# Kernel tuning notes

Measured on AMD Instinct MI355X. Metric: run time of the kernel, lower is better.

## Reference

```python
import jax, jax.numpy as jnp
import numpy as np

N, E = 50000, 1_600_000
IN_DIM, OUT_DIM, E_IN, E_OUT = 128, 64, 32, 32


def setup_inputs() -> dict:
    key = jax.random.key(0)
    ks = jax.random.split(key, 8)
    h = jax.random.normal(ks[0], (N, IN_DIM), jnp.float32)
    edge_w = jax.random.normal(ks[1], (E, E_IN), jnp.float32)
    src = jax.random.randint(ks[2], (E,), 0, N)
    dst = jax.random.randint(ks[3], (E,), 0, N)

    def winit(k, shape):
        fan_in = shape[0]
        return jax.random.normal(k, shape, jnp.float32) / np.float32(np.sqrt(fan_in))

    W_node = winit(ks[4], (IN_DIM, OUT_DIM))
    W_attn = winit(ks[5], (2 * OUT_DIM + E_IN, 1))
    W_tonode = winit(ks[6], (OUT_DIM + E_IN, OUT_DIM))
    W_edge = winit(ks[7], (2 * OUT_DIM + E_IN, E_OUT))
    return dict(h=h, edge_w=edge_w, W_node=W_node, W_attn=W_attn,
                W_tonode=W_tonode, W_edge=W_edge, src=src, dst=dst)


def reference(h, edge_w, W_node, W_attn, W_tonode, W_edge, src, dst):
    n = h.shape[0]
    d = W_node.shape[1]

    # embed_node
    z = h @ W_node                      # [N, D]
    zs = z[src]                         # [E, D] gather (message source feats)
    zd = z[dst]                         # [E, D]

    # edge_attention: attn_fc(cat[src, dst, w]) == split-matmul sum (no concat)
    a = zs @ W_attn[:d] + zd @ W_attn[d:2 * d] + edge_w @ W_attn[2 * d:]  # [E,1]
    e = jax.nn.leaky_relu(a, negative_slope=0.1)[:, 0]                    # [E]

    # segment softmax over incoming edges of each dst node
    emax = jax.lax.stop_gradient(jax.ops.segment_max(e, dst, num_segments=n))
    ex = jnp.exp(e - emax[dst])
    denom = jax.ops.segment_sum(ex, dst, num_segments=n)
    alpha = ex / denom[dst]             # [E]

    # to_node_fc(cat[src_h, w]) then alpha-weighted segment sum
    t = zs @ W_tonode[:d] + edge_w @ W_tonode[d:]         # [E, D]
    h_agg = jax.ops.segment_sum(alpha[:, None] * t, dst, num_segments=n)

    # DGL: zero-in-degree nodes keep embed_node output
    indeg = jax.ops.segment_sum(jnp.ones_like(e), dst, num_segments=n)
    h_new = jnp.where(indeg[:, None] > 0, h_agg, z)       # [N, D]

    # edge_calc on UPDATED node features
    w_new = (h_new[src] @ W_edge[:d] + h_new[dst] @ W_edge[d:2 * d]
             + edge_w @ W_edge[2 * d:])                   # [E, E_OUT]
    return h_new, w_new
```

## Files before the change

### kernel.cpp

```cpp
#include <hip/hip_runtime.h>

#define N_NODES 50000
#define N_EDGES 1600000
#define IN_DIM  128
#define D       64
#define E_IN    32
#define E_OUT   32
#define SCAN_CHUNK 256
#define N_CHUNKS ((N_NODES + SCAN_CHUNK - 1) / SCAN_CHUNK)

typedef __attribute__((ext_vector_type(4))) float f32x4;

__global__ __launch_bounds__(256) void node_a_kernel(
    const float* __restrict__ h, const float* __restrict__ Wn,
    const float* __restrict__ Wa, const float* __restrict__ Wt,
    float* __restrict__ z, float* __restrict__ u,
    float* __restrict__ s1, float* __restrict__ s2)
{
    __shared__ float lWn[IN_DIM * D];
    __shared__ float lWt1[D * D];
    __shared__ float lWa[2 * D];
    __shared__ float lh[4][IN_DIM];
    __shared__ float lz[4][D];

    const int tid = threadIdx.x;
    for (int i = tid; i < IN_DIM * D; i += 256) lWn[i] = Wn[i];
    for (int i = tid; i < D * D; i += 256) lWt1[i] = Wt[i];
    if (tid < 2 * D) lWa[tid] = Wa[tid];
    __syncthreads();

    const int wid = tid >> 6;
    const int lane = tid & 63;
    const int nwaves = gridDim.x * 4;

    for (int n = blockIdx.x * 4 + wid; n < N_NODES; n += nwaves) {
        lh[wid][lane]      = h[(size_t)n * IN_DIM + lane];
        lh[wid][lane + 64] = h[(size_t)n * IN_DIM + 64 + lane];

        float acc = 0.f;
        #pragma unroll 8
        for (int k = 0; k < IN_DIM; ++k)
            acc = fmaf(lh[wid][k], lWn[k * D + lane], acc);
        z[(size_t)n * D + lane] = acc;
        lz[wid][lane] = acc;

        float p1 = acc * lWa[lane];
        float p2 = acc * lWa[D + lane];
        #pragma unroll
        for (int off = 32; off > 0; off >>= 1) {
            p1 += __shfl_xor(p1, off, 64);
            p2 += __shfl_xor(p2, off, 64);
        }
        if (lane == 0) { s1[n] = p1; s2[n] = p2; }

        float ua = 0.f;
        #pragma unroll 8
        for (int k = 0; k < D; ++k)
            ua = fmaf(lz[wid][k], lWt1[k * D + lane], ua);
        u[(size_t)n * D + lane] = ua;
    }
}

__global__ __launch_bounds__(256) void hist_kernel(
    const int* __restrict__ dst, int* __restrict__ count)
{
    int i = blockIdx.x * 256 + threadIdx.x;
    const int stride = gridDim.x * 256;
    for (; i < N_EDGES; i += stride) atomicAdd(&count[dst[i]], 1);
}

__global__ __launch_bounds__(256) void scan_sum_kernel(
    const int* __restrict__ count, int* __restrict__ bsum)
{
    __shared__ int s[256];
    const int t = threadIdx.x;
    const int idx = blockIdx.x * 256 + t;
    s[t] = (idx < N_NODES) ? count[idx] : 0;
    __syncthreads();
    for (int off = 128; off > 0; off >>= 1) {
        if (t < off) s[t] += s[t + off];
        __syncthreads();
    }
    if (t == 0) bsum[blockIdx.x] = s[0];
}

__global__ __launch_bounds__(256) void scan_top_kernel(int* __restrict__ bsum)
{
    __shared__ int s[256];
    const int t = threadIdx.x;
    const int v = (t < N_CHUNKS) ? bsum[t] : 0;
    s[t] = v;
    __syncthreads();
    for (int off = 1; off < 256; off <<= 1) {
        int x = (t >= off) ? s[t - off] : 0;
        __syncthreads();
        s[t] += x;
        __syncthreads();
    }
    if (t < N_CHUNKS) bsum[t] = s[t] - v;
}

__global__ __launch_bounds__(256) void scan_local_kernel(
    const int* __restrict__ count, const int* __restrict__ bsum,
    int* __restrict__ offsets, int* __restrict__ cursor)
{
    __shared__ int s[256];
    const int t = threadIdx.x;
    const int idx = blockIdx.x * 256 + t;
    const int v = (idx < N_NODES) ? count[idx] : 0;
    s[t] = v;
    __syncthreads();
    for (int off = 1; off < 256; off <<= 1) {
        int x = (t >= off) ? s[t - off] : 0;
        __syncthreads();
        s[t] += x;
        __syncthreads();
    }
    if (idx < N_NODES) {
        int e = bsum[blockIdx.x] + s[t] - v;
        offsets[idx] = e;
        cursor[idx]  = e;
    }
}

__global__ __launch_bounds__(256) void scatter_ex_kernel(
    const float* __restrict__ edge_w, const int* __restrict__ src,
    const int* __restrict__ dst, const float* __restrict__ Wa,
    const float* __restrict__ s1, const float* __restrict__ s2,
    int* __restrict__ cursor, int* __restrict__ pe, int* __restrict__ ps,
    float* __restrict__ exs)
{
    float wa[E_IN];
    #pragma unroll
    for (int k = 0; k < E_IN; ++k) wa[k] = Wa[2 * D + k];

    int i = blockIdx.x * 256 + threadIdx.x;
    const int stride = gridDim.x * 256;
    for (; i < N_EDGES; i += stride) {
        const int s = src[i];
        const int d = dst[i];
        float a = s1[s] + s2[d];
        const float4* r4 = (const float4*)(edge_w + (size_t)i * E_IN);
        #pragma unroll
        for (int qq = 0; qq < E_IN / 4; ++qq) {
            float4 v = r4[qq];
            a = fmaf(v.x, wa[4 * qq + 0], a);
            a = fmaf(v.y, wa[4 * qq + 1], a);
            a = fmaf(v.z, wa[4 * qq + 2], a);
            a = fmaf(v.w, wa[4 * qq + 3], a);
        }
        const float lk = (a > 0.f) ? a : 0.1f * a;
        const float ex = __expf(lk);
        const int pos = atomicAdd(&cursor[d], 1);
        pe[pos]  = i;
        ps[pos]  = s;
        exs[pos] = ex;
    }
}

__global__ __launch_bounds__(256) void edge_a_sorted_kernel(
    const float* __restrict__ edge_w,
    const int* __restrict__ pe, const int* __restrict__ ps,
    const float* __restrict__ exs,
    const int* __restrict__ offsets, const int* __restrict__ count,
    const float* __restrict__ Wt, const float* __restrict__ We,
    const float* __restrict__ u, const float* __restrict__ z,
    float* __restrict__ hout, float* __restrict__ p, float* __restrict__ q)
{
    __shared__ float lWE[D * 64];
    __shared__ float lh[4][D];
    __shared__ float lrr[4][E_IN];
    const int tid = threadIdx.x;
    for (int i = tid; i < D * 64; i += 256) {
        int j = i >> 6, l = i & 63;
        lWE[i] = We[(j + ((l < 32) ? 0 : D)) * E_OUT + (l & 31)];
    }
    __syncthreads();

    const int wid = tid >> 6, lane = tid & 63;
    const int nwaves = gridDim.x * 4;

    float wt2r[E_IN];
    #pragma unroll
    for (int k = 0; k < E_IN; ++k)
        wt2r[k] = Wt[(D + k) * D + lane];

    for (int n = blockIdx.x * 4 + wid; n < N_NODES; n += nwaves) {
        const int off = offsets[n];
        const int deg = count[n];
        float g = 0.f, rv = 0.f, denv = 0.f;

        for (int b = 0; b < deg; b += 64) {
            int rem = deg - b; if (rem > 64) rem = 64;
            int eb = 0, sb = 0; float exv = 0.f;
            if (lane < rem) {
                eb  = pe[off + b + lane];
                sb  = ps[off + b + lane];
                exv = exs[off + b + lane];
            }
            denv += exv;
            const int rem4 = (rem + 3) & ~3;
            for (int i = 0; i < rem4; i += 4) {
                const int s0 = __builtin_amdgcn_readlane(sb, i);
                const int s1 = __builtin_amdgcn_readlane(sb, i + 1);
                const int s2 = __builtin_amdgcn_readlane(sb, i + 2);
                const int s3 = __builtin_amdgcn_readlane(sb, i + 3);
                const int e0 = __builtin_amdgcn_readlane(eb, i);
                const int e1 = __builtin_amdgcn_readlane(eb, i + 1);
                const int e2 = __builtin_amdgcn_readlane(eb, i + 2);
                const int e3 = __builtin_amdgcn_readlane(eb, i + 3);
                const float x0 = __int_as_float(__builtin_amdgcn_readlane(__float_as_int(exv), i));
                const float x1 = __int_as_float(__builtin_amdgcn_readlane(__float_as_int(exv), i + 1));
                const float x2 = __int_as_float(__builtin_amdgcn_readlane(__float_as_int(exv), i + 2));
                const float x3 = __int_as_float(__builtin_amdgcn_readlane(__float_as_int(exv), i + 3));
                const float u0 = u[(size_t)s0 * D + lane];
                const float u1 = u[(size_t)s1 * D + lane];
                const float u2 = u[(size_t)s2 * D + lane];
                const float u3 = u[(size_t)s3 * D + lane];
                const int   ea = (lane < 32) ? e0 : e1;
                const float xa = (lane < 32) ? x0 : x1;
                const int   ec = (lane < 32) ? e2 : e3;
                const float xc = (lane < 32) ? x2 : x3;
                const float w0 = edge_w[(size_t)ea * E_IN + (lane & 31)];
                const float w1 = edge_w[(size_t)ec * E_IN + (lane & 31)];
                g  = fmaf(x0, u0, g);
                g  = fmaf(x1, u1, g);
                g  = fmaf(x2, u2, g);
                g  = fmaf(x3, u3, g);
                rv = fmaf(xa, w0, rv);
                rv = fmaf(xc, w1, rv);
            }
        }

        rv += __shfl_xor(rv, 32, 64);
        if (lane < 32) lrr[wid][lane] = rv;
        #pragma unroll
        for (int o = 32; o > 0; o >>= 1) denv += __shfl_xor(denv, o, 64);

        float acc = g;
        #pragma unroll
        for (int k = 0; k < E_IN; ++k)
            acc = fmaf(lrr[wid][k], wt2r[k], acc);

        const float hv = (deg > 0) ? acc / denv : z[(size_t)n * D + lane];
        hout[(size_t)n * D + lane] = hv;
        lh[wid][lane] = hv;

        float pacc = 0.f;
        #pragma unroll 8
        for (int j = 0; j < D; ++j)
            pacc = fmaf(lh[wid][j], lWE[j * 64 + lane], pacc);

        float* o = (lane < 32) ? p : q;
        o[(size_t)n * E_OUT + (lane & 31)] = pacc;
    }
}

__global__ __launch_bounds__(256) void edge_b_kernel(
    const float* __restrict__ edge_w, const int* __restrict__ src,
    const int* __restrict__ dst, const float* __restrict__ We,
    const float* __restrict__ p, const float* __restrict__ q,
    float* __restrict__ wout)
{
    const int lane = threadIdx.x & 63;
    const int ic   = lane & 31;
    const int half = lane >> 5;
    const int g0   = blockIdx.x * 4 + (threadIdx.x >> 6);
    const int ngroups = N_EDGES / 8;
    const int nw   = gridDim.x * 4;

    float we3r[E_IN];
    #pragma unroll
    for (int k = 0; k < E_IN; ++k) we3r[k] = We[(2 * D + k) * E_OUT + ic];

    if (g0 >= ngroups) return;

    int s[4], d[4];
    #pragma unroll
    for (int i = 0; i < 4; ++i) {
        const int e = g0 * 8 + 2 * i + half;
        s[i] = src[e];
        d[i] = dst[e];
    }

    for (int g = g0; g < ngroups; g += nw) {
        const int ebase = g * 8;
        const int gn = g + nw;

        float pv[4], qv[4];
        #pragma unroll
        for (int i = 0; i < 4; ++i) pv[i] = p[(size_t)s[i] * E_OUT + ic];
        #pragma unroll
        for (int i = 0; i < 4; ++i) qv[i] = q[(size_t)d[i] * E_OUT + ic];

        if (gn < ngroups) {
            #pragma unroll
            for (int i = 0; i < 4; ++i) {
                const int e = gn * 8 + 2 * i + half;
                s[i] = src[e];
                d[i] = dst[e];
            }
        }

        float acc[4];
        #pragma unroll
        for (int i = 0; i < 4; ++i) acc[i] = 0.f;
        #pragma unroll
        for (int qq = 0; qq < E_IN / 4; ++qq) {
            f32x4 v[4];
            #pragma unroll
            for (int i = 0; i < 4; ++i) {
                const int e = ebase + 2 * i + half;
                const f32x4* ew4 = (const f32x4*)(edge_w + (size_t)e * E_IN);
                v[i] = __builtin_nontemporal_load(&ew4[qq]);
            }
            #pragma unroll
            for (int i = 0; i < 4; ++i) {
                acc[i] = fmaf(v[i].x, we3r[4 * qq + 0], acc[i]);
                acc[i] = fmaf(v[i].y, we3r[4 * qq + 1], acc[i]);
                acc[i] = fmaf(v[i].z, we3r[4 * qq + 2], acc[i]);
                acc[i] = fmaf(v[i].w, we3r[4 * qq + 3], acc[i]);
            }
        }

        #pragma unroll
        for (int i = 0; i < 4; ++i) acc[i] += pv[i] + qv[i];

        #pragma unroll
        for (int i = 0; i < 4; ++i) {
            const int e = ebase + 2 * i + half;
            __builtin_nontemporal_store(acc[i], &wout[(size_t)e * E_OUT + ic]);
        }
    }
}

extern "C" void kernel_launch(void* const* d_in, const int* in_sizes, int n_in,
                              void* d_out, int out_size, void* d_ws, size_t ws_size,
                              hipStream_t stream) {
    const float* h  = (const float*)d_in[0];
    const float* ew = (const float*)d_in[1];
    const float* Wn = (const float*)d_in[2];
    const float* Wa = (const float*)d_in[3];
    const float* Wt = (const float*)d_in[4];
    const float* We = (const float*)d_in[5];
    const int* src  = (const int*)d_in[6];
    const int* dst  = (const int*)d_in[7];

    float* z    = (float*)d_ws;
    float* u    = z + (size_t)N_NODES * D;
    float* s1   = u + (size_t)N_NODES * D;
    float* s2   = s1 + N_NODES;
    float* p    = s2 + N_NODES;
    float* q    = p + (size_t)N_NODES * E_OUT;
    int* counts = (int*)(q + (size_t)N_NODES * E_OUT);
    int* offs   = counts + N_NODES;
    int* cursor = offs + N_NODES;
    int* bsum   = cursor + N_NODES;
    int* pe     = bsum + 256;
    int* ps     = pe + N_EDGES;
    float* exs  = (float*)(ps + N_EDGES);

    float* hout = (float*)d_out;
    float* wout = hout + (size_t)N_NODES * D;

    hipMemsetAsync(counts, 0, N_NODES * sizeof(int), stream);

    node_a_kernel<<<1024, 256, 0, stream>>>(h, Wn, Wa, Wt, z, u, s1, s2);
    hist_kernel<<<1024, 256, 0, stream>>>(dst, counts);
    scan_sum_kernel<<<N_CHUNKS, 256, 0, stream>>>(counts, bsum);
    scan_top_kernel<<<1, 256, 0, stream>>>(bsum);
    scan_local_kernel<<<N_CHUNKS, 256, 0, stream>>>(counts, bsum, offs, cursor);
    scatter_ex_kernel<<<2048, 256, 0, stream>>>(ew, src, dst, Wa, s1, s2,
                                                cursor, pe, ps, exs);
    edge_a_sorted_kernel<<<2048, 256, 0, stream>>>(ew, pe, ps, exs, offs, counts,
                                                   Wt, We, u, z, hout, p, q);
    edge_b_kernel<<<2048, 256, 0, stream>>>(ew, src, dst, We, p, q, wout);
}
```

Before: 993.1 us.

## Software-pipeline gathers in node aggregation and edge output kernels

The node aggregation loop now double-buffers its per-edge work: the u and edge_w gathers for the next four edges are issued before the FMAs for the current four, processing eight edges per iteration. The edge output kernel prefetches p/q gathers and src/dst indices two groups ahead with ping-pong register sets, so the dependent gathers overlap with the edge_w MLP of the current group. Both changes aim to hide random-gather latency and raise memory-level parallelism. In exchange they use more VGPRs, which may lower occupancy.

```diff
diff --git a/kernel.cpp b/kernel.cpp
--- a/kernel.cpp
+++ b/kernel.cpp
@@ -10,6 +10,10 @@
 #define N_CHUNKS ((N_NODES + SCAN_CHUNK - 1) / SCAN_CHUNK)
 
 typedef __attribute__((ext_vector_type(4))) float f32x4;
+
+__device__ __forceinline__ float rlanef(float v, int l) {
+    return __int_as_float(__builtin_amdgcn_readlane(__float_as_int(v), l));
+}
 
 __global__ __launch_bounds__(256) void node_a_kernel(
     const float* __restrict__ h, const float* __restrict__ Wn,
@@ -179,6 +183,7 @@
 
     const int wid = tid >> 6, lane = tid & 63;
     const int nwaves = gridDim.x * 4;
+    const bool lo = (lane < 32);
 
     float wt2r[E_IN];
     #pragma unroll
@@ -199,36 +204,80 @@
                 exv = exs[off + b + lane];
             }
             denv += exv;
-            const int rem4 = (rem + 3) & ~3;
-            for (int i = 0; i < rem4; i += 4) {
-                const int s0 = __builtin_amdgcn_readlane(sb, i);
-                const int s1 = __builtin_amdgcn_readlane(sb, i + 1);
-                const int s2 = __builtin_amdgcn_readlane(sb, i + 2);
-                const int s3 = __builtin_amdgcn_readlane(sb, i + 3);
-                const int e0 = __builtin_amdgcn_readlane(eb, i);
-                const int e1 = __builtin_amdgcn_readlane(eb, i + 1);
-                const int e2 = __builtin_amdgcn_readlane(eb, i + 2);
-                const int e3 = __builtin_amdgcn_readlane(eb, i + 3);
-                const float x0 = __int_as_float(__builtin_amdgcn_readlane(__float_as_int(exv), i));
-                const float x1 = __int_as_float(__builtin_amdgcn_readlane(__float_as_int(exv), i + 1));
-                const float x2 = __int_as_float(__builtin_amdgcn_readlane(__float_as_int(exv), i + 2));
-                const float x3 = __int_as_float(__builtin_amdgcn_readlane(__float_as_int(exv), i + 3));
-                const float u0 = u[(size_t)s0 * D + lane];
-                const float u1 = u[(size_t)s1 * D + lane];
-                const float u2 = u[(size_t)s2 * D + lane];
-                const float u3 = u[(size_t)s3 * D + lane];
-                const int   ea = (lane < 32) ? e0 : e1;
-                const float xa = (lane < 32) ? x0 : x1;
-                const int   ec = (lane < 32) ? e2 : e3;
-                const float xc = (lane < 32) ? x2 : x3;
-                const float w0 = edge_w[(size_t)ea * E_IN + (lane & 31)];
-                const float w1 = edge_w[(size_t)ec * E_IN + (lane & 31)];
-                g  = fmaf(x0, u0, g);
-                g  = fmaf(x1, u1, g);
-                g  = fmaf(x2, u2, g);
-                g  = fmaf(x3, u3, g);
-                rv = fmaf(xa, w0, rv);
-                rv = fmaf(xc, w1, rv);
+            const int rem8 = (rem + 7) & ~7;
+
+            int sA0 = __builtin_amdgcn_readlane(sb, 0);
+            int sA1 = __builtin_amdgcn_readlane(sb, 1);
+            int sA2 = __builtin_amdgcn_readlane(sb, 2);
+            int sA3 = __builtin_amdgcn_readlane(sb, 3);
+            int eA0 = __builtin_amdgcn_readlane(eb, 0);
+            int eA1 = __builtin_amdgcn_readlane(eb, 1);
+            int eA2 = __builtin_amdgcn_readlane(eb, 2);
+            int eA3 = __builtin_amdgcn_readlane(eb, 3);
+            float xA0 = rlanef(exv, 0), xA1 = rlanef(exv, 1);
+            float xA2 = rlanef(exv, 2), xA3 = rlanef(exv, 3);
+            float uA0 = u[(size_t)sA0 * D + lane];
+            float uA1 = u[(size_t)sA1 * D + lane];
+            float uA2 = u[(size_t)sA2 * D + lane];
+            float uA3 = u[(size_t)sA3 * D + lane];
+            float wA0 = edge_w[(size_t)(lo ? eA0 : eA1) * E_IN + (lane & 31)];
+            float wA1 = edge_w[(size_t)(lo ? eA2 : eA3) * E_IN + (lane & 31)];
+            float xAa = lo ? xA0 : xA1, xAc = lo ? xA2 : xA3;
+
+            for (int i = 0; i < rem8; i += 8) {
+                const int jb = i + 4;
+                int sB0 = __builtin_amdgcn_readlane(sb, jb);
+                int sB1 = __builtin_amdgcn_readlane(sb, jb + 1);
+                int sB2 = __builtin_amdgcn_readlane(sb, jb + 2);
+                int sB3 = __builtin_amdgcn_readlane(sb, jb + 3);
+                int eB0 = __builtin_amdgcn_readlane(eb, jb);
+                int eB1 = __builtin_amdgcn_readlane(eb, jb + 1);
+                int eB2 = __builtin_amdgcn_readlane(eb, jb + 2);
+                int eB3 = __builtin_amdgcn_readlane(eb, jb + 3);
+                float xB0 = rlanef(exv, jb),     xB1 = rlanef(exv, jb + 1);
+                float xB2 = rlanef(exv, jb + 2), xB3 = rlanef(exv, jb + 3);
+                float uB0 = u[(size_t)sB0 * D + lane];
+                float uB1 = u[(size_t)sB1 * D + lane];
+                float uB2 = u[(size_t)sB2 * D + lane];
+                float uB3 = u[(size_t)sB3 * D + lane];
+                float wB0 = edge_w[(size_t)(lo ? eB0 : eB1) * E_IN + (lane & 31)];
+                float wB1 = edge_w[(size_t)(lo ? eB2 : eB3) * E_IN + (lane & 31)];
+                float xBa = lo ? xB0 : xB1, xBc = lo ? xB2 : xB3;
+
+                g  = fmaf(xA0, uA0, g);
+                g  = fmaf(xA1, uA1, g);
+                g  = fmaf(xA2, uA2, g);
+                g  = fmaf(xA3, uA3, g);
+                rv = fmaf(xAa, wA0, rv);
+                rv = fmaf(xAc, wA1, rv);
+
+                if (i + 8 < rem8) {
+                    const int ja = i + 8;
+                    sA0 = __builtin_amdgcn_readlane(sb, ja);
+                    sA1 = __builtin_amdgcn_readlane(sb, ja + 1);
+                    sA2 = __builtin_amdgcn_readlane(sb, ja + 2);
+                    sA3 = __builtin_amdgcn_readlane(sb, ja + 3);
+                    eA0 = __builtin_amdgcn_readlane(eb, ja);
+                    eA1 = __builtin_amdgcn_readlane(eb, ja + 1);
+                    eA2 = __builtin_amdgcn_readlane(eb, ja + 2);
+                    eA3 = __builtin_amdgcn_readlane(eb, ja + 3);
+                    xA0 = rlanef(exv, ja);     xA1 = rlanef(exv, ja + 1);
+                    xA2 = rlanef(exv, ja + 2); xA3 = rlanef(exv, ja + 3);
+                    uA0 = u[(size_t)sA0 * D + lane];
+                    uA1 = u[(size_t)sA1 * D + lane];
+                    uA2 = u[(size_t)sA2 * D + lane];
+                    uA3 = u[(size_t)sA3 * D + lane];
+                    wA0 = edge_w[(size_t)(lo ? eA0 : eA1) * E_IN + (lane & 31)];
+                    wA1 = edge_w[(size_t)(lo ? eA2 : eA3) * E_IN + (lane & 31)];
+                    xAa = lo ? xA0 : xA1; xAc = lo ? xA2 : xA3;
+                }
+
+                g  = fmaf(xB0, uB0, g);
+                g  = fmaf(xB1, uB1, g);
+                g  = fmaf(xB2, uB2, g);
+                g  = fmaf(xB3, uB3, g);
+                rv = fmaf(xBa, wB0, rv);
+                rv = fmaf(xBc, wB1, rv);
             }
         }
 
@@ -253,6 +302,31 @@
 
         float* o = (lane < 32) ? p : q;
         o[(size_t)n * E_OUT + (lane & 31)] = pacc;
+    }
+}
+
+__device__ __forceinline__ void ew_mlp4(const float* __restrict__ edge_w,
+                                        int ebase, int half,
+                                        const float* we3r, float* acc)
+{
+    #pragma unroll
+    for (int i = 0; i < 4; ++i) acc[i] = 0.f;
+    #pragma unroll
+    for (int qq = 0; qq < E_IN / 4; ++qq) {
+        f32x4 v[4];
+        #pragma unroll
+        for (int i = 0; i < 4; ++i) {
+            const int e = ebase + 2 * i + half;
+            const f32x4* ew4 = (const f32x4*)(edge_w + (size_t)e * E_IN);
+            v[i] = __builtin_nontemporal_load(&ew4[qq]);
+        }
+        #pragma unroll
+        for (int i = 0; i < 4; ++i) {
+            acc[i] = fmaf(v[i].x, we3r[4 * qq + 0], acc[i]);
+            acc[i] = fmaf(v[i].y, we3r[4 * qq + 1], acc[i]);
+            acc[i] = fmaf(v[i].z, we3r[4 * qq + 2], acc[i]);
+            acc[i] = fmaf(v[i].w, we3r[4 * qq + 3], acc[i]);
+        }
     }
 }
 
@@ -273,64 +347,86 @@
     #pragma unroll
     for (int k = 0; k < E_IN; ++k) we3r[k] = We[(2 * D + k) * E_OUT + ic];
 
-    if (g0 >= ngroups) return;
-
-    int s[4], d[4];
+    int gA = g0;
+    if (gA >= ngroups) return;
+
+    int sA[4], dA[4], sB[4], dB[4];
     #pragma unroll
     for (int i = 0; i < 4; ++i) {
-        const int e = g0 * 8 + 2 * i + half;
-        s[i] = src[e];
-        d[i] = dst[e];
-    }
-
-    for (int g = g0; g < ngroups; g += nw) {
-        const int ebase = g * 8;
-        const int gn = g + nw;
-
-        float pv[4], qv[4];
-        #pragma unroll
-        for (int i = 0; i < 4; ++i) pv[i] = p[(size_t)s[i] * E_OUT + ic];
-        #pragma unroll
-        for (int i = 0; i < 4; ++i) qv[i] = q[(size_t)d[i] * E_OUT + ic];
-
-        if (gn < ngroups) {
+        const int e = gA * 8 + 2 * i + half;
+        sA[i] = src[e]; dA[i] = dst[e];
+    }
+    float pvA[4], qvA[4], pvB[4], qvB[4];
+    #pragma unroll
+    for (int i = 0; i < 4; ++i) pvA[i] = p[(size_t)sA[i] * E_OUT + ic];
+    #pragma unroll
+    for (int i = 0; i < 4; ++i) qvA[i] = q[(size_t)dA[i] * E_OUT + ic];
+
+    int gB = gA + nw;
+    if (gB < ngroups) {
+        #pragma unroll
+        for (int i = 0; i < 4; ++i) {
+            const int e = gB * 8 + 2 * i + half;
+            sB[i] = src[e]; dB[i] = dst[e];
+        }
+    }
+
+    while (true) {
+        if (gB < ngroups) {
+            #pragma unroll
+            for (int i = 0; i < 4; ++i) pvB[i] = p[(size_t)sB[i] * E_OUT + ic];
+            #pragma unroll
+            for (int i = 0; i < 4; ++i) qvB[i] = q[(size_t)dB[i] * E_OUT + ic];
+        }
+        const int gC = gB + nw;
+        if (gC < ngroups) {
             #pragma unroll
             for (int i = 0; i < 4; ++i) {
-                const int e = gn * 8 + 2 * i + half;
-                s[i] = src[e];
-                d[i] = dst[e];
-            }
-        }
-
-        float acc[4];
-        #pragma unroll
-        for (int i = 0; i < 4; ++i) acc[i] = 0.f;
-        #pragma unroll
-        for (int qq = 0; qq < E_IN / 4; ++qq) {
-            f32x4 v[4];
+                const int e = gC * 8 + 2 * i + half;
+                sA[i] = src[e]; dA[i] = dst[e];
+            }
+        }
+        {
+            float acc[4];
+            ew_mlp4(edge_w, gA * 8, half, we3r, acc);
+            #pragma unroll
+            for (int i = 0; i < 4; ++i) acc[i] += pvA[i] + qvA[i];
             #pragma unroll
             for (int i = 0; i < 4; ++i) {
-                const int e = ebase + 2 * i + half;
-                const f32x4* ew4 = (const f32x4*)(edge_w + (size_t)e * E_IN);
-                v[i] = __builtin_nontemporal_load(&ew4[qq]);
-            }
+                const int e = gA * 8 + 2 * i + half;
+                __builtin_nontemporal_store(acc[i], &wout[(size_t)e * E_OUT + ic]);
+            }
+        }
+        if (gB >= ngroups) break;
+
+        if (gC < ngroups) {
+            #pragma unroll
+            for (int i = 0; i < 4; ++i) pvA[i] = p[(size_t)sA[i] * E_OUT + ic];
+            #pragma unroll
+            for (int i = 0; i < 4; ++i) qvA[i] = q[(size_t)dA[i] * E_OUT + ic];
+        }
+        const int gD = gC + nw;
+        if (gD < ngroups) {
             #pragma unroll
             for (int i = 0; i < 4; ++i) {
-                acc[i] = fmaf(v[i].x, we3r[4 * qq + 0], acc[i]);
-                acc[i] = fmaf(v[i].y, we3r[4 * qq + 1], acc[i]);
-                acc[i] = fmaf(v[i].z, we3r[4 * qq + 2], acc[i]);
-                acc[i] = fmaf(v[i].w, we3r[4 * qq + 3], acc[i]);
-            }
-        }
-
-        #pragma unroll
-        for (int i = 0; i < 4; ++i) acc[i] += pv[i] + qv[i];
-
-        #pragma unroll
-        for (int i = 0; i < 4; ++i) {
-            const int e = ebase + 2 * i + half;
-            __builtin_nontemporal_store(acc[i], &wout[(size_t)e * E_OUT + ic]);
-        }
+                const int e = gD * 8 + 2 * i + half;
+                sB[i] = src[e]; dB[i] = dst[e];
+            }
+        }
+        {
+            float acc[4];
+            ew_mlp4(edge_w, gB * 8, half, we3r, acc);
+            #pragma unroll
+            for (int i = 0; i < 4; ++i) acc[i] += pvB[i] + qvB[i];
+            #pragma unroll
+            for (int i = 0; i < 4; ++i) {
+                const int e = gB * 8 + 2 * i + half;
+                __builtin_nontemporal_store(acc[i], &wout[(size_t)e * E_OUT + ic]);
+            }
+        }
+        if (gC >= ngroups) break;
+
+        gA = gC; gB = gD;
     }
 }
 
```

New measurement: 973.1 us. 2.0% less time.
